# Kernel tuning notes

Measured on AMD Instinct MI355X. Metric: run time of the kernel, lower is better.

The kernel has to match this reference:

```python
import jax, jax.numpy as jnp
import numpy as np

D_MODEL = 1024
NUM_HEADS = 16
D_K = D_MODEL // NUM_HEADS
LN_EPS = 1e-5


def setup_inputs() -> dict:
    key = jax.random.key(0)
    ks = jax.random.split(key, 10)
    s = 1.0 / np.sqrt(D_MODEL)
    x = jax.random.normal(ks[0], (4, 2048, D_MODEL), dtype=jnp.float32)
    Wq = jax.random.uniform(ks[1], (D_MODEL, D_MODEL), jnp.float32, -s, s)
    bq = jax.random.uniform(ks[2], (D_MODEL,), jnp.float32, -s, s)
    Wk = jax.random.uniform(ks[3], (D_MODEL, D_MODEL), jnp.float32, -s, s)
    bk = jax.random.uniform(ks[4], (D_MODEL,), jnp.float32, -s, s)
    Wv = jax.random.uniform(ks[5], (D_MODEL, D_MODEL), jnp.float32, -s, s)
    bv = jax.random.uniform(ks[6], (D_MODEL,), jnp.float32, -s, s)
    Wo = jax.random.uniform(ks[7], (D_MODEL, D_MODEL), jnp.float32, -s, s)
    bo = jax.random.uniform(ks[8], (D_MODEL,), jnp.float32, -s, s)
    gamma = jnp.ones((D_MODEL,), jnp.float32)
    beta = jnp.zeros((D_MODEL,), jnp.float32)
    return {"x": x, "Wq": Wq, "bq": bq, "Wk": Wk, "bk": bk, "Wv": Wv,
            "bv": bv, "Wo": Wo, "bo": bo, "gamma": gamma, "beta": beta}


def reference(x, Wq, bq, Wk, bk, Wv, bv, Wo, bo, gamma, beta):
    B, S, D = x.shape
    H, dk = NUM_HEADS, D_K
    # torch Linear: y = x @ W.T + b
    def proj(W, b):
        y = jnp.einsum('bsd,ed->bse', x, W) + b
        return y.reshape(B, S, H, dk).transpose(0, 2, 1, 3)  # [B,H,S,dk]
    Q = proj(Wq, bq)
    K = proj(Wk, bk)
    V = proj(Wv, bv)
    scores = jnp.einsum('bhqd,bhkd->bhqk', Q, K) / np.sqrt(dk)
    attn = jax.nn.softmax(scores, axis=-1)
    head = jnp.einsum('bhqk,bhkd->bhqd', attn, V)
    head = head.transpose(0, 2, 1, 3).reshape(B, S, D)
    out = jnp.einsum('bsd,ed->bse', head, Wo) + bo
    # LayerNorm
    mu = jnp.mean(out, axis=-1, keepdims=True)
    var = jnp.var(out, axis=-1, keepdims=True)
    out = (out - mu) * jax.lax.rsqrt(var + LN_EPS) * gamma + beta
    # dropout is identity in eval mode
    return x + out
```

## Files before the change

### kernel.cpp

```cpp
#include <hip/hip_runtime.h>
#include <stdint.h>

typedef unsigned short u16;
typedef unsigned int u32;
typedef __attribute__((ext_vector_type(8))) short short8;
typedef __attribute__((ext_vector_type(4))) short short4b;
typedef __attribute__((ext_vector_type(4))) float f32x4;
typedef __attribute__((ext_vector_type(4))) unsigned short u16x4;

#define DEV static __device__ __forceinline__

DEV float bf2f(u16 b) { return __uint_as_float(((uint32_t)b) << 16); }
DEV u16 f2bf(float f) {
  uint32_t u = __float_as_uint(f);
  u += 0x7FFFu + ((u >> 16) & 1u);
  return (u16)(u >> 16);
}
DEV void gld16(const u16* gsrc, u16* ldsdst) {
  __builtin_amdgcn_global_load_lds((const __attribute__((address_space(1))) void*)gsrc,
                                   (__attribute__((address_space(3))) void*)ldsdst, 16, 0, 0);
}
#define MFMA16(a, b, c) __builtin_amdgcn_mfma_f32_16x16x32_bf16(a, b, c, 0, 0, 0)

#if __has_builtin(__builtin_amdgcn_mfma_f32_16x16x16bf16_1k)
DEV f32x4 mfma_k16(short4b a, short4b b, f32x4 c) {
  return __builtin_amdgcn_mfma_f32_16x16x16bf16_1k(a, b, c, 0, 0, 0);
}
#else
DEV f32x4 mfma_k16(short4b a, short4b b, f32x4 c) {
  f32x4 d;
  asm volatile("v_mfma_f32_16x16x16_bf16 %0, %1, %2, %3"
               : "=&v"(d) : "v"(a), "v"(b), "v"(c));
  return d;
}
#endif

#if __has_builtin(__builtin_amdgcn_exp2f)
DEV float fexp2(float x) { return __builtin_amdgcn_exp2f(x); }
#else
DEV float fexp2(float x) { return exp2f(x); }
#endif

DEV u32 cvtpk(float lo, float hi) {
  u32 r;
  asm("v_cvt_pk_bf16_f32 %0, %1, %2" : "=v"(r) : "v"(lo), "v"(hi));
  return r;
}

DEV f32x4 v4max(f32x4 a, f32x4 b) {
  f32x4 r;
  r.x = fmaxf(a.x, b.x); r.y = fmaxf(a.y, b.y);
  r.z = fmaxf(a.z, b.z); r.w = fmaxf(a.w, b.w);
  return r;
}

__global__ __launch_bounds__(256) void k_convert(
    const float* __restrict__ x, const float* __restrict__ wq, const float* __restrict__ wk,
    const float* __restrict__ wv, const float* __restrict__ wo, u16* __restrict__ ws)
{
  int bid = blockIdx.x, t = threadIdx.x;
  const float* src; u16* dst; size_t off;
  if (bid < 8192) { src = x; dst = ws; off = (size_t)bid * 1024; }
  else {
    int r = bid - 8192; int sel = r >> 10; int lb = r & 1023;
    src = sel == 0 ? wq : sel == 1 ? wk : sel == 2 ? wv : wo;
    dst = ws + 8388608u + (size_t)sel * 1048576u;
    off = (size_t)lb * 1024;
  }
  size_t e = off + (size_t)t * 4;
  f32x4 v = *(const f32x4*)(src + e);
  u16x4 o;
  o.x = f2bf(v.x); o.y = f2bf(v.y); o.z = f2bf(v.z); o.w = f2bf(v.w);
  *(u16x4*)(dst + e) = o;
}

DEV void gemm_mainloop(const u16* __restrict__ A, const u16* __restrict__ B,
                       int m0, int n0, u16* As, u16* Bs, f32x4 acc[4][4])
{
  const int tid = threadIdx.x, lane = tid & 63, w = tid >> 6;
  const int fr = lane & 15, g = lane >> 4;
  const int wm = w >> 1, wn = w & 1;

  const int rowA0 = (w * 2 + 0) * 16 + (lane >> 2);
  const int rowA1 = (w * 2 + 1) * 16 + (lane >> 2);
  const int ci = lane & 3;
  const u16* ga0 = A + (size_t)(m0 + rowA0) * 1024 + ((ci ^ (rowA0 & 3)) << 3);
  const u16* ga1 = A + (size_t)(m0 + rowA1) * 1024 + ((ci ^ (rowA1 & 3)) << 3);
  const u16* gb0 = B + (size_t)(n0 + rowA0) * 1024 + ((ci ^ (rowA0 & 3)) << 3);
  const u16* gb1 = B + (size_t)(n0 + rowA1) * 1024 + ((ci ^ (rowA1 & 3)) << 3);
  u16* lA0 = As + (w * 2 + 0) * 512;
  u16* lA1 = As + (w * 2 + 1) * 512;
  u16* lB0 = Bs + (w * 2 + 0) * 512;
  u16* lB1 = Bs + (w * 2 + 1) * 512;

  int raf[4], rbf[4];
#pragma unroll
  for (int i = 0; i < 4; ++i) {
    int rA = wm * 64 + i * 16 + fr;
    raf[i] = rA * 32 + ((g ^ (rA & 3)) << 3);
    int rB = wn * 64 + i * 16 + fr;
    rbf[i] = rB * 32 + ((g ^ (rB & 3)) << 3);
  }

  for (int k0 = 0; k0 < 1024; k0 += 32) {
    __syncthreads();
    gld16(ga0 + k0, lA0);
    gld16(ga1 + k0, lA1);
    gld16(gb0 + k0, lB0);
    gld16(gb1 + k0, lB1);
    __syncthreads();
    short8 af[4], bf[4];
#pragma unroll
    for (int i = 0; i < 4; ++i) af[i] = *(const short8*)&As[raf[i]];
#pragma unroll
    for (int i = 0; i < 4; ++i) bf[i] = *(const short8*)&Bs[rbf[i]];
#pragma unroll
    for (int mi = 0; mi < 4; ++mi)
#pragma unroll
      for (int ni = 0; ni < 4; ++ni)
        acc[mi][ni] = MFMA16(af[mi], bf[ni], acc[mi][ni]);
  }
}

__global__ __launch_bounds__(256) void k_gemm_qkv(
    const u16* __restrict__ xb, const u16* __restrict__ wqb, const u16* __restrict__ wkb,
    const u16* __restrict__ wvb, const float* __restrict__ bq, const float* __restrict__ bk,
    const float* __restrict__ bv, u16* __restrict__ Qg, u16* __restrict__ Kg,
    u16* __restrict__ Vtg)
{
  __shared__ u16 As[128 * 32], Bs[128 * 32];
  const int mb = blockIdx.x, nb_all = blockIdx.y;
  const int mat = nb_all >> 3, nb = nb_all & 7;
  const u16* W = mat == 0 ? wqb : (mat == 1 ? wkb : wvb);
  const float* bias = mat == 0 ? bq : (mat == 1 ? bk : bv);
  const int m0 = mb * 128, n0 = nb * 128;

  f32x4 acc[4][4];
  f32x4 z = {0.f, 0.f, 0.f, 0.f};
#pragma unroll
  for (int i = 0; i < 4; ++i)
#pragma unroll
    for (int j = 0; j < 4; ++j) acc[i][j] = z;

  gemm_mainloop(xb, W, m0, n0, As, Bs, acc);

  const int tid = threadIdx.x, lane = tid & 63, w = tid >> 6;
  const int fr = lane & 15, g = lane >> 4;
  const int wm = w >> 1, wn = w & 1;

  if (mat <= 1) {
    u16* Og = mat == 0 ? Qg : Kg;
    const float scale = mat == 0 ? 0.18033688011112042f : 1.0f;
#pragma unroll
    for (int mi = 0; mi < 4; ++mi)
#pragma unroll
      for (int ni = 0; ni < 4; ++ni) {
        int n = n0 + wn * 64 + ni * 16 + fr;
        float bv_ = bias[n];
        int h = n >> 6, d = n & 63;
#pragma unroll
        for (int r = 0; r < 4; ++r) {
          int m = m0 + wm * 64 + mi * 16 + 4 * g + r;
          int b = m >> 11, s = m & 2047;
          float v = (acc[mi][ni][r] + bv_) * scale;
          Og[(((size_t)(b * 16 + h)) * 2048 + (size_t)s) * 64 + d] = f2bf(v);
        }
      }
  } else {
#pragma unroll
    for (int mi = 0; mi < 4; ++mi)
#pragma unroll
      for (int ni = 0; ni < 4; ++ni) {
        int n = n0 + wn * 64 + ni * 16 + fr;
        float bv_ = bias[n];
        int h = n >> 6, d = n & 63;
        int mbase = m0 + wm * 64 + mi * 16 + 4 * g;
        int b = mbase >> 11, s0 = mbase & 2047;
        u16x4 pk;
        pk.x = f2bf(acc[mi][ni][0] + bv_);
        pk.y = f2bf(acc[mi][ni][1] + bv_);
        pk.z = f2bf(acc[mi][ni][2] + bv_);
        pk.w = f2bf(acc[mi][ni][3] + bv_);
        *(u16x4*)&Vtg[(((size_t)(b * 16 + h)) * 64 + d) * 2048 + s0] = pk;
      }
  }
}

__global__ __launch_bounds__(256, 3) void k_attn(
    const u16* __restrict__ Qg, const u16* __restrict__ Kg, const u16* __restrict__ Vtg,
    u16* __restrict__ headb)
{
  __shared__ u16 K_lds[128 * 64];
  __shared__ u16 V_lds[64 * 128];
  const int tid = threadIdx.x, lane = tid & 63, w = tid >> 6;
  const int fr = lane & 15, g = lane >> 4;
  const int qb = blockIdx.x, bh = blockIdx.y;
  const u16* Qbase = Qg + (size_t)bh * 2048 * 64;
  const u16* Kbase = Kg + (size_t)bh * 2048 * 64;
  const u16* Vbase = Vtg + (size_t)bh * 64 * 2048;

  short8 qf[2][2];
#pragma unroll
  for (int mi = 0; mi < 2; ++mi)
#pragma unroll
    for (int kt = 0; kt < 2; ++kt) {
      int qrow = qb * 128 + w * 32 + mi * 16 + fr;
      qf[mi][kt] = *(const short8*)&Qbase[(size_t)qrow * 64 + kt * 32 + g * 8];
    }

  f32x4 po[2][4];
  f32x4 z = {0.f, 0.f, 0.f, 0.f};
#pragma unroll
  for (int mi = 0; mi < 2; ++mi)
#pragma unroll
    for (int dt = 0; dt < 4; ++dt) po[mi][dt] = z;
  float mrun[2] = {-1e30f, -1e30f};
  float lrun[2] = {0.f, 0.f};

  for (int kv = 0; kv < 16; ++kv) {
    __syncthreads();
#pragma unroll
    for (int i = 0; i < 4; ++i) {
      int c = w * 4 + i;
      int row = c * 8 + (lane >> 3);
      int ci = lane & 7;
      gld16(Kbase + ((size_t)(kv * 128 + row)) * 64 + ((ci ^ (row & 7)) << 3), &K_lds[c * 512]);
    }
#pragma unroll
    for (int i = 0; i < 4; ++i) {
      int c = w * 4 + i;
      int row = c * 4 + (lane >> 4);
      int ci = lane & 15;
      gld16(Vbase + (size_t)row * 2048 + kv * 128 + ((ci ^ (row & 7)) << 3), &V_lds[c * 512]);
    }
    __syncthreads();

    f32x4 sc[2][8];
#pragma unroll
    for (int mi = 0; mi < 2; ++mi)
#pragma unroll
      for (int nt = 0; nt < 8; ++nt) sc[mi][nt] = z;
#pragma unroll
    for (int nt = 0; nt < 8; ++nt) {
      int rk = nt * 16 + fr;
#pragma unroll
      for (int kt = 0; kt < 2; ++kt) {
        short8 kb = *(const short8*)&K_lds[rk * 64 + (((kt * 4 + g) ^ (rk & 7)) << 3)];
        sc[0][nt] = MFMA16(kb, qf[0][kt], sc[0][nt]);
        sc[1][nt] = MFMA16(kb, qf[1][kt], sc[1][nt]);
      }
    }

    short4b pa[2][8];
#pragma unroll
    for (int mi = 0; mi < 2; ++mi) {
      f32x4 m4 = sc[mi][0];
#pragma unroll
      for (int nt = 1; nt < 8; ++nt) m4 = v4max(m4, sc[mi][nt]);
      float mx = fmaxf(fmaxf(m4.x, m4.y), fmaxf(m4.z, m4.w));
      mx = fmaxf(mx, __shfl_xor(mx, 16, 64));
      mx = fmaxf(mx, __shfl_xor(mx, 32, 64));
      float mnew = fmaxf(mrun[mi], mx);
      float alpha = fexp2(mrun[mi] - mnew);
      f32x4 s4 = z;
#pragma unroll
      for (int nt = 0; nt < 8; ++nt) {
        f32x4 p;
        p.x = fexp2(sc[mi][nt].x - mnew);
        p.y = fexp2(sc[mi][nt].y - mnew);
        p.z = fexp2(sc[mi][nt].z - mnew);
        p.w = fexp2(sc[mi][nt].w - mnew);
        sc[mi][nt] = p;
        s4 += p;
      }
      float rs = (s4.x + s4.y) + (s4.z + s4.w);
      rs += __shfl_xor(rs, 16, 64);
      rs += __shfl_xor(rs, 32, 64);
      lrun[mi] = lrun[mi] * alpha + rs;
      mrun[mi] = mnew;
      f32x4 al4;
#pragma unroll
      for (int r = 0; r < 4; ++r) al4[r] = __shfl(alpha, 4 * g + r, 64);
#pragma unroll
      for (int dt = 0; dt < 4; ++dt) po[mi][dt] *= al4;
#pragma unroll
      for (int nt = 0; nt < 8; ++nt) {
        union { u32 u[2]; short4b s; } cv;
        cv.u[0] = cvtpk(sc[mi][nt].x, sc[mi][nt].y);
        cv.u[1] = cvtpk(sc[mi][nt].z, sc[mi][nt].w);
        pa[mi][nt] = cv.s;
      }
    }

#pragma unroll
    for (int nt = 0; nt < 8; ++nt) {
#pragma unroll
      for (int dt = 0; dt < 4; ++dt) {
        int d = dt * 16 + fr;
        short4b vb = *(const short4b*)&V_lds[d * 128 + ((((nt << 1) | (g >> 1)) ^ (d & 7)) << 3) + ((g & 1) << 2)];
        po[0][dt] = mfma_k16(pa[0][nt], vb, po[0][dt]);
        po[1][dt] = mfma_k16(pa[1][nt], vb, po[1][dt]);
      }
    }
  }

  float linv[2][4];
#pragma unroll
  for (int mi = 0; mi < 2; ++mi)
#pragma unroll
    for (int r = 0; r < 4; ++r)
      linv[mi][r] = 1.0f / __shfl(lrun[mi], 4 * g + r, 64);

  const int b = bh >> 4, h = bh & 15;
#pragma unroll
  for (int mi = 0; mi < 2; ++mi)
#pragma unroll
    for (int dt = 0; dt < 4; ++dt)
#pragma unroll
      for (int r = 0; r < 4; ++r) {
        int srow = qb * 128 + w * 32 + mi * 16 + 4 * g + r;
        float v = po[mi][dt][r] * linv[mi][r];
        int e = h * 64 + dt * 16 + fr;
        headb[((size_t)(b * 2048 + srow)) * 1024 + e] = f2bf(v);
      }
}

__global__ __launch_bounds__(256) void k_gemm_o(
    const u16* __restrict__ headb, const u16* __restrict__ wob, const float* __restrict__ bo,
    u16* __restrict__ projb)
{
  __shared__ u16 As[128 * 32], Bs[128 * 32];
  const int m0 = blockIdx.x * 128, n0 = blockIdx.y * 128;
  f32x4 acc[4][4];
  f32x4 z = {0.f, 0.f, 0.f, 0.f};
#pragma unroll
  for (int i = 0; i < 4; ++i)
#pragma unroll
    for (int j = 0; j < 4; ++j) acc[i][j] = z;

  gemm_mainloop(headb, wob, m0, n0, As, Bs, acc);

  const int tid = threadIdx.x, lane = tid & 63, w = tid >> 6;
  const int fr = lane & 15, g = lane >> 4;
  const int wm = w >> 1, wn = w & 1;
#pragma unroll
  for (int mi = 0; mi < 4; ++mi)
#pragma unroll
    for (int ni = 0; ni < 4; ++ni) {
      int n = n0 + wn * 64 + ni * 16 + fr;
      float bv_ = bo[n];
#pragma unroll
      for (int r = 0; r < 4; ++r) {
        int m = m0 + wm * 64 + mi * 16 + 4 * g + r;
        projb[(size_t)m * 1024 + n] = f2bf(acc[mi][ni][r] + bv_);
      }
    }
}

__global__ __launch_bounds__(256) void k_ln(
    const u16* __restrict__ projb, const float* __restrict__ x,
    const float* __restrict__ gamma, const float* __restrict__ beta, float* __restrict__ out)
{
  __shared__ float sh1[4], sh2[4];
  const int row = blockIdx.x, t = threadIdx.x, lane = t & 63, w = t >> 6;
  const size_t base = (size_t)row * 1024;
  u16x4 pv = *(const u16x4*)&projb[base + t * 4];
  float v0 = bf2f(pv.x), v1 = bf2f(pv.y), v2 = bf2f(pv.z), v3 = bf2f(pv.w);
  float s1 = v0 + v1 + v2 + v3;
  float s2 = v0 * v0 + v1 * v1 + v2 * v2 + v3 * v3;
  for (int m = 1; m < 64; m <<= 1) {
    s1 += __shfl_xor(s1, m, 64);
    s2 += __shfl_xor(s2, m, 64);
  }
  if (lane == 0) { sh1[w] = s1; sh2[w] = s2; }
  __syncthreads();
  s1 = sh1[0] + sh1[1] + sh1[2] + sh1[3];
  s2 = sh2[0] + sh2[1] + sh2[2] + sh2[3];
  float mu = s1 * (1.0f / 1024.0f);
  float var = s2 * (1.0f / 1024.0f) - mu * mu;
  float rsd = rsqrtf(var + 1e-5f);
  f32x4 xv = *(const f32x4*)&x[base + t * 4];
  f32x4 res;
  int e = t * 4;
  res.x = xv.x + (v0 - mu) * rsd * gamma[e + 0] + beta[e + 0];
  res.y = xv.y + (v1 - mu) * rsd * gamma[e + 1] + beta[e + 1];
  res.z = xv.z + (v2 - mu) * rsd * gamma[e + 2] + beta[e + 2];
  res.w = xv.w + (v3 - mu) * rsd * gamma[e + 3] + beta[e + 3];
  *(f32x4*)&out[base + t * 4] = res;
}

extern "C" void kernel_launch(void* const* d_in, const int* in_sizes, int n_in,
                              void* d_out, int out_size, void* d_ws, size_t ws_size,
                              hipStream_t stream)
{
  const float* x     = (const float*)d_in[0];
  const float* Wq    = (const float*)d_in[1];
  const float* bq    = (const float*)d_in[2];
  const float* Wk    = (const float*)d_in[3];
  const float* bk    = (const float*)d_in[4];
  const float* Wv    = (const float*)d_in[5];
  const float* bv    = (const float*)d_in[6];
  const float* Wo    = (const float*)d_in[7];
  const float* bo    = (const float*)d_in[8];
  const float* gamma = (const float*)d_in[9];
  const float* beta  = (const float*)d_in[10];
  float* out = (float*)d_out;

  u16* ws   = (u16*)d_ws;
  u16* xb   = ws;
  u16* wqb  = ws + 8388608;
  u16* wkb  = wqb + 1048576;
  u16* wvb  = wkb + 1048576;
  u16* wob  = wvb + 1048576;
  u16* Qg   = wob + 1048576;
  u16* Kg   = Qg + 8388608;
  u16* Vtg  = Kg + 8388608;
  u16* headb = Vtg + 8388608;
  u16* projb = Qg;

  k_convert<<<12288, 256, 0, stream>>>(x, Wq, Wk, Wv, Wo, ws);
  k_gemm_qkv<<<dim3(64, 24), 256, 0, stream>>>(xb, wqb, wkb, wvb, bq, bk, bv, Qg, Kg, Vtg);
  k_attn<<<dim3(16, 64), 256, 0, stream>>>(Qg, Kg, Vtg, headb);
  k_gemm_o<<<dim3(64, 8), 256, 0, stream>>>(headb, wob, bo, projb);
  k_ln<<<8192, 256, 0, stream>>>(projb, x, gamma, beta, out);
}
```

Baseline: 240.0 us.

## Double-buffer LDS tiles in GEMM and attention, widen attention blocks to 512 threads

Both GEMM mainloops and the attention kernel now use two LDS buffers, so the next K-tile's global-to-LDS loads are issued before computing on the current one. The two full __syncthreads per iteration become explicit vmcnt waits plus raw barriers. Attention blocks grow to 512 threads covering 256 query rows, which halves the number of times each K/V tile is loaded per head and spreads the tile load across 8 waves. LDS use doubles, which may lower occupancy, and the hand-written vmcnt counts must match the number of loads each thread issues.

```diff
diff --git a/kernel.cpp b/kernel.cpp
--- a/kernel.cpp
+++ b/kernel.cpp
@@ -21,6 +21,14 @@
                                    (__attribute__((address_space(3))) void*)ldsdst, 16, 0, 0);
 }
 #define MFMA16(a, b, c) __builtin_amdgcn_mfma_f32_16x16x32_bf16(a, b, c, 0, 0, 0)
+
+#define WAITVM4() asm volatile("s_waitcnt vmcnt(4)" ::: "memory")
+#define WAITVM0() asm volatile("s_waitcnt vmcnt(0)" ::: "memory")
+DEV void barrier() {
+  asm volatile("" ::: "memory");
+  __builtin_amdgcn_s_barrier();
+  asm volatile("" ::: "memory");
+}
 
 #if __has_builtin(__builtin_amdgcn_mfma_f32_16x16x16bf16_1k)
 DEV f32x4 mfma_k16(short4b a, short4b b, f32x4 c) {
@@ -75,7 +83,8 @@
 }
 
 DEV void gemm_mainloop(const u16* __restrict__ A, const u16* __restrict__ B,
-                       int m0, int n0, u16* As, u16* Bs, f32x4 acc[4][4])
+                       int m0, int n0, u16 (*As)[128 * 32], u16 (*Bs)[128 * 32],
+                       f32x4 acc[4][4])
 {
   const int tid = threadIdx.x, lane = tid & 63, w = tid >> 6;
   const int fr = lane & 15, g = lane >> 4;
@@ -88,10 +97,7 @@
   const u16* ga1 = A + (size_t)(m0 + rowA1) * 1024 + ((ci ^ (rowA1 & 3)) << 3);
   const u16* gb0 = B + (size_t)(n0 + rowA0) * 1024 + ((ci ^ (rowA0 & 3)) << 3);
   const u16* gb1 = B + (size_t)(n0 + rowA1) * 1024 + ((ci ^ (rowA1 & 3)) << 3);
-  u16* lA0 = As + (w * 2 + 0) * 512;
-  u16* lA1 = As + (w * 2 + 1) * 512;
-  u16* lB0 = Bs + (w * 2 + 0) * 512;
-  u16* lB1 = Bs + (w * 2 + 1) * 512;
+  const int lo0 = (w * 2 + 0) * 512, lo1 = (w * 2 + 1) * 512;
 
   int raf[4], rbf[4];
 #pragma unroll
@@ -102,23 +108,38 @@
     rbf[i] = rB * 32 + ((g ^ (rB & 3)) << 3);
   }
 
-  for (int k0 = 0; k0 < 1024; k0 += 32) {
-    __syncthreads();
-    gld16(ga0 + k0, lA0);
-    gld16(ga1 + k0, lA1);
-    gld16(gb0 + k0, lB0);
-    gld16(gb1 + k0, lB1);
-    __syncthreads();
+  gld16(ga0, As[0] + lo0);
+  gld16(ga1, As[0] + lo1);
+  gld16(gb0, Bs[0] + lo0);
+  gld16(gb1, Bs[0] + lo1);
+
+  for (int t = 0; t < 32; ++t) {
+    const int cur = t & 1;
+    if (t < 31) {
+      const int k1 = (t + 1) * 32;
+      gld16(ga0 + k1, As[cur ^ 1] + lo0);
+      gld16(ga1 + k1, As[cur ^ 1] + lo1);
+      gld16(gb0 + k1, Bs[cur ^ 1] + lo0);
+      gld16(gb1 + k1, Bs[cur ^ 1] + lo1);
+      WAITVM4();
+    } else {
+      WAITVM0();
+    }
+    barrier();
+    const u16* Ab = As[cur];
+    const u16* Bb = Bs[cur];
     short8 af[4], bf[4];
 #pragma unroll
-    for (int i = 0; i < 4; ++i) af[i] = *(const short8*)&As[raf[i]];
-#pragma unroll
-    for (int i = 0; i < 4; ++i) bf[i] = *(const short8*)&Bs[rbf[i]];
+    for (int i = 0; i < 4; ++i) af[i] = *(const short8*)&Ab[raf[i]];
+#pragma unroll
+    for (int i = 0; i < 4; ++i) bf[i] = *(const short8*)&Bs[cur][rbf[i]];
 #pragma unroll
     for (int mi = 0; mi < 4; ++mi)
 #pragma unroll
       for (int ni = 0; ni < 4; ++ni)
         acc[mi][ni] = MFMA16(af[mi], bf[ni], acc[mi][ni]);
+    barrier();
+    (void)Bb;
   }
 }
 
@@ -128,7 +149,7 @@
     const float* __restrict__ bv, u16* __restrict__ Qg, u16* __restrict__ Kg,
     u16* __restrict__ Vtg)
 {
-  __shared__ u16 As[128 * 32], Bs[128 * 32];
+  __shared__ u16 As[2][128 * 32], Bs[2][128 * 32];
   const int mb = blockIdx.x, nb_all = blockIdx.y;
   const int mat = nb_all >> 3, nb = nb_all & 7;
   const u16* W = mat == 0 ? wqb : (mat == 1 ? wkb : wvb);
@@ -186,12 +207,12 @@
   }
 }
 
-__global__ __launch_bounds__(256, 3) void k_attn(
+__global__ __launch_bounds__(512, 4) void k_attn(
     const u16* __restrict__ Qg, const u16* __restrict__ Kg, const u16* __restrict__ Vtg,
     u16* __restrict__ headb)
 {
-  __shared__ u16 K_lds[128 * 64];
-  __shared__ u16 V_lds[64 * 128];
+  __shared__ u16 K_lds[2][128 * 64];
+  __shared__ u16 V_lds[2][64 * 128];
   const int tid = threadIdx.x, lane = tid & 63, w = tid >> 6;
   const int fr = lane & 15, g = lane >> 4;
   const int qb = blockIdx.x, bh = blockIdx.y;
@@ -199,12 +220,22 @@
   const u16* Kbase = Kg + (size_t)bh * 2048 * 64;
   const u16* Vbase = Vtg + (size_t)bh * 64 * 2048;
 
+  const int ck0 = w * 2, ck1 = w * 2 + 1;
+  const int krow0 = ck0 * 8 + (lane >> 3), krow1 = ck1 * 8 + (lane >> 3);
+  const int kci = lane & 7;
+  const u16* gk0 = Kbase + (size_t)krow0 * 64 + ((kci ^ (krow0 & 7)) << 3);
+  const u16* gk1 = Kbase + (size_t)krow1 * 64 + ((kci ^ (krow1 & 7)) << 3);
+  const int vrow0 = ck0 * 4 + (lane >> 4), vrow1 = ck1 * 4 + (lane >> 4);
+  const int vci = lane & 15;
+  const u16* gv0 = Vbase + (size_t)vrow0 * 2048 + ((vci ^ (vrow0 & 7)) << 3);
+  const u16* gv1 = Vbase + (size_t)vrow1 * 2048 + ((vci ^ (vrow1 & 7)) << 3);
+
   short8 qf[2][2];
 #pragma unroll
   for (int mi = 0; mi < 2; ++mi)
 #pragma unroll
     for (int kt = 0; kt < 2; ++kt) {
-      int qrow = qb * 128 + w * 32 + mi * 16 + fr;
+      int qrow = qb * 256 + w * 32 + mi * 16 + fr;
       qf[mi][kt] = *(const short8*)&Qbase[(size_t)qrow * 64 + kt * 32 + g * 8];
     }
 
@@ -217,23 +248,27 @@
   float mrun[2] = {-1e30f, -1e30f};
   float lrun[2] = {0.f, 0.f};
 
+  gld16(gk0, K_lds[0] + ck0 * 512);
+  gld16(gk1, K_lds[0] + ck1 * 512);
+  gld16(gv0, V_lds[0] + ck0 * 512);
+  gld16(gv1, V_lds[0] + ck1 * 512);
+
   for (int kv = 0; kv < 16; ++kv) {
-    __syncthreads();
-#pragma unroll
-    for (int i = 0; i < 4; ++i) {
-      int c = w * 4 + i;
-      int row = c * 8 + (lane >> 3);
-      int ci = lane & 7;
-      gld16(Kbase + ((size_t)(kv * 128 + row)) * 64 + ((ci ^ (row & 7)) << 3), &K_lds[c * 512]);
-    }
-#pragma unroll
-    for (int i = 0; i < 4; ++i) {
-      int c = w * 4 + i;
-      int row = c * 4 + (lane >> 4);
-      int ci = lane & 15;
-      gld16(Vbase + (size_t)row * 2048 + kv * 128 + ((ci ^ (row & 7)) << 3), &V_lds[c * 512]);
-    }
-    __syncthreads();
+    const int cur = kv & 1;
+    if (kv < 15) {
+      const int ko = (kv + 1) * 128 * 64;
+      const int vo = (kv + 1) * 128;
+      gld16(gk0 + ko, K_lds[cur ^ 1] + ck0 * 512);
+      gld16(gk1 + ko, K_lds[cur ^ 1] + ck1 * 512);
+      gld16(gv0 + vo, V_lds[cur ^ 1] + ck0 * 512);
+      gld16(gv1 + vo, V_lds[cur ^ 1] + ck1 * 512);
+      WAITVM4();
+    } else {
+      WAITVM0();
+    }
+    barrier();
+    const u16* Kc = K_lds[cur];
+    const u16* Vc = V_lds[cur];
 
     f32x4 sc[2][8];
 #pragma unroll
@@ -245,7 +280,7 @@
       int rk = nt * 16 + fr;
 #pragma unroll
       for (int kt = 0; kt < 2; ++kt) {
-        short8 kb = *(const short8*)&K_lds[rk * 64 + (((kt * 4 + g) ^ (rk & 7)) << 3)];
+        short8 kb = *(const short8*)&Kc[rk * 64 + (((kt * 4 + g) ^ (rk & 7)) << 3)];
         sc[0][nt] = MFMA16(kb, qf[0][kt], sc[0][nt]);
         sc[1][nt] = MFMA16(kb, qf[1][kt], sc[1][nt]);
       }
@@ -297,11 +332,12 @@
 #pragma unroll
       for (int dt = 0; dt < 4; ++dt) {
         int d = dt * 16 + fr;
-        short4b vb = *(const short4b*)&V_lds[d * 128 + ((((nt << 1) | (g >> 1)) ^ (d & 7)) << 3) + ((g & 1) << 2)];
+        short4b vb = *(const short4b*)&Vc[d * 128 + ((((nt << 1) | (g >> 1)) ^ (d & 7)) << 3) + ((g & 1) << 2)];
         po[0][dt] = mfma_k16(pa[0][nt], vb, po[0][dt]);
         po[1][dt] = mfma_k16(pa[1][nt], vb, po[1][dt]);
       }
     }
+    barrier();
   }
 
   float linv[2][4];
@@ -318,7 +354,7 @@
     for (int dt = 0; dt < 4; ++dt)
 #pragma unroll
       for (int r = 0; r < 4; ++r) {
-        int srow = qb * 128 + w * 32 + mi * 16 + 4 * g + r;
+        int srow = qb * 256 + w * 32 + mi * 16 + 4 * g + r;
         float v = po[mi][dt][r] * linv[mi][r];
         int e = h * 64 + dt * 16 + fr;
         headb[((size_t)(b * 2048 + srow)) * 1024 + e] = f2bf(v);
@@ -329,7 +365,7 @@
     const u16* __restrict__ headb, const u16* __restrict__ wob, const float* __restrict__ bo,
     u16* __restrict__ projb)
 {
-  __shared__ u16 As[128 * 32], Bs[128 * 32];
+  __shared__ u16 As[2][128 * 32], Bs[2][128 * 32];
   const int m0 = blockIdx.x * 128, n0 = blockIdx.y * 128;
   f32x4 acc[4][4];
   f32x4 z = {0.f, 0.f, 0.f, 0.f};
@@ -420,7 +456,7 @@
 
   k_convert<<<12288, 256, 0, stream>>>(x, Wq, Wk, Wv, Wo, ws);
   k_gemm_qkv<<<dim3(64, 24), 256, 0, stream>>>(xb, wqb, wkb, wvb, bq, bk, bv, Qg, Kg, Vtg);
-  k_attn<<<dim3(16, 64), 256, 0, stream>>>(Qg, Kg, Vtg, headb);
+  k_attn<<<dim3(8, 64), 512, 0, stream>>>(Qg, Kg, Vtg, headb);
   k_gemm_o<<<dim3(64, 8), 256, 0, stream>>>(headb, wob, bo, projb);
   k_ln<<<8192, 256, 0, stream>>>(projb, x, gamma, beta, out);
 }
```

New measurement: 333.4 us. 1.39x slower.
